# Performance work log

Hardware: AMD Instinct MI355X
Metric: run time of the kernel (lower is better)

Reference implementation:

```python
import jax, jax.numpy as jnp
import numpy as np

B, N, W, R = 32, 1024, 128, 4
EPS = 1e-8  # torch CosineSimilarity eps


def _cosine(key, mem):
    # key: (B,K,W), mem: (B,N,W) -> (B,K,N); torch-style eps clamp on norm product
    dot = jnp.einsum('bkw,bnw->bkn', key, mem)
    kn = jnp.linalg.norm(key, axis=-1)[..., None]          # (B,K,1)
    mn = jnp.linalg.norm(mem, axis=-1)[:, None, :]          # (B,1,N)
    return dot / jnp.maximum(kn * mn, EPS)


def setup_inputs() -> dict:
    key = jax.random.key(0)
    ks = jax.random.split(key, 16)
    inp = {
        'memory': jax.random.normal(ks[0], (B, N, W), jnp.float32) * 0.1,
        'temporal_link': jax.random.uniform(ks[1], (B, N, N), jnp.float32) / N,
        'usage': jax.random.uniform(ks[2], (B, 1, N), jnp.float32),
        'precedence': jax.random.uniform(ks[3], (B, 1, N), jnp.float32) / N,
        'read_weights': jax.nn.softmax(jax.random.normal(ks[4], (B, R, N), jnp.float32), axis=-1),
        'read_keys': jax.random.normal(ks[5], (B, R, W), jnp.float32),
        'read_strength': 1.0 + jax.random.uniform(ks[6], (B, R, 1), jnp.float32),
        'read_modes': jax.nn.softmax(jax.random.normal(ks[7], (B, R, 3), jnp.float32), axis=-1),
        'write_key': jax.random.normal(ks[8], (B, W), jnp.float32),
        'write_strength': 1.0 + jax.random.uniform(ks[9], (B, 1), jnp.float32),
        'allocation_gate': jax.random.uniform(ks[10], (B, 1, 1), jnp.float32),
        'write_gate': jax.random.uniform(ks[11], (B, 1, 1), jnp.float32),
        'write_vector': jax.random.normal(ks[12], (B, 1, W), jnp.float32),
        'erase_vector': jax.random.uniform(ks[13], (B, 1, W), jnp.float32),
        'free_gates': jax.random.uniform(ks[14], (B, R, 1), jnp.float32),
    }
    return inp


def reference(memory, temporal_link, usage, precedence, read_weights,
              read_keys, read_strength, read_modes, write_key, write_strength,
              allocation_gate, write_gate, write_vector, erase_vector, free_gates):
    # --- read weights: temporal (fwd/bwd) + content modes ---
    # NOTE: source softmaxes the raw cosine, THEN multiplies by strength
    content_r = jax.nn.softmax(_cosine(read_keys, memory), axis=-1) * read_strength  # (B,R,N)
    fw = jnp.einsum('brn,bmn->brm', read_weights, temporal_link)   # rw @ L^T
    bw = jnp.einsum('brn,bnm->brm', read_weights, temporal_link)   # rw @ L
    new_rw = (fw * read_modes[:, :, 0:1] + bw * read_modes[:, :, 1:2]
              + content_r * read_modes[:, :, 2:3])                 # (B,R,N)
    read_result = jnp.einsum('brn,bnw->brw', new_rw, memory)       # (B,R,W)

    # --- allocation: exclusive cumprod of (unsorted) usage, as in source ---
    cp = jnp.cumprod(usage, axis=-1)
    excl = jnp.concatenate([jnp.ones_like(cp[..., :1]), cp[..., :-1]], axis=-1)
    allocation = (1.0 - usage) * excl                              # (B,1,N)

    # --- write weights (source multiplies strength BEFORE softmax here) ---
    wc = jax.nn.softmax(_cosine(write_key[:, None, :], memory)
                        * write_strength[:, :, None], axis=-1)     # (B,1,N)
    ww = (allocation_gate * (allocation - wc) + wc) * write_gate   # (B,1,N)
    wwT = jnp.swapaxes(ww, 1, 2)                                   # (B,N,1)

    # --- memory erase/write (outer products via broadcasting) ---
    memory_new = memory * (1.0 - wwT * erase_vector) + wwT * write_vector

    # --- temporal link update ---
    grid = wwT + ww                                                # (B,N,N)
    link_new = (1.0 - grid) * temporal_link + wwT * precedence     # (B,N,N)

    # NOTE: source uses a GLOBAL scalar sum of write weights here
    precedence_new = (1.0 - jnp.sum(ww)) * precedence + ww

    # --- usage update (source uses the freshly updated read weights) ---
    retention = jnp.prod(1.0 - free_gates * new_rw, axis=1, keepdims=True)  # (B,1,N)
    usage_new = (usage + ww - usage * ww) * retention

    return (read_result, memory_new, link_new, usage_new, precedence_new, new_rw)
```

## Files before the change

### kernel.cpp

```cpp
#include <hip/hip_runtime.h>
#include <math.h>

#define B 32
#define N 1024
#define W 128
#define R 4
#define EPSC 1e-8f

typedef float f32x4 __attribute__((ext_vector_type(4)));

#define WS_SUM   0
#define WS_BW    64
#define WS_FW    (WS_BW + B*16*R*N)
#define WS_CONT  (WS_FW + B*R*N)
#define WS_COSR  (WS_CONT + B*R*N)
#define WS_COSW  (WS_COSR + B*R*N)
#define WS_WW    (WS_COSW + B*N)

#define O_RR    0
#define O_MEM   (O_RR + B*R*W)
#define O_LINK  (O_MEM + B*N*W)
#define O_USAGE (O_LINK + B*N*N)
#define O_PREC  (O_USAGE + B*N)
#define O_NRW   (O_PREC + B*N)

__global__ void k1_scores(const float* __restrict__ mem,
                          const float* __restrict__ rkeys,
                          const float* __restrict__ wkey,
                          float* __restrict__ ws) {
    int bx = blockIdx.x;
    int b = bx >> 6;
    int n0 = (bx & 63) << 4;
    int t = threadIdx.x;
    __shared__ float keys[5][W];
    __shared__ float knorm[5];
    for (int idx = t; idx < 5 * W; idx += 256) {
        int r = idx >> 7, w = idx & 127;
        keys[r][w] = (r < 4) ? rkeys[(b * R + r) * W + w] : wkey[b * W + w];
    }
    __syncthreads();
    if (t < 160) {
        int kidx = t >> 5, l = t & 31;
        float s = 0.f;
        #pragma unroll
        for (int c = 0; c < 4; ++c) { float v = keys[kidx][l * 4 + c]; s += v * v; }
        #pragma unroll
        for (int st = 1; st <= 16; st <<= 1) s += __shfl_xor(s, st);
        if (l == 0) knorm[kidx] = sqrtf(s);
    }
    __syncthreads();
    int l16 = t & 15;
    int rloc = t >> 4;
    int n = n0 + rloc;
    const float* mrow = mem + ((size_t)(b * N + n)) * W + l16 * 8;
    float4 a  = *reinterpret_cast<const float4*>(mrow);
    float4 a2 = *reinterpret_cast<const float4*>(mrow + 4);
    float mm = a.x*a.x + a.y*a.y + a.z*a.z + a.w*a.w
             + a2.x*a2.x + a2.y*a2.y + a2.z*a2.z + a2.w*a2.w;
    float d[5];
    #pragma unroll
    for (int r = 0; r < 5; ++r) {
        float4 k1v = *reinterpret_cast<const float4*>(&keys[r][l16 * 8]);
        float4 k2v = *reinterpret_cast<const float4*>(&keys[r][l16 * 8 + 4]);
        d[r] = a.x*k1v.x + a.y*k1v.y + a.z*k1v.z + a.w*k1v.w
             + a2.x*k2v.x + a2.y*k2v.y + a2.z*k2v.z + a2.w*k2v.w;
    }
    #pragma unroll
    for (int st = 1; st <= 8; st <<= 1) {
        mm += __shfl_xor(mm, st);
        #pragma unroll
        for (int r = 0; r < 5; ++r) d[r] += __shfl_xor(d[r], st);
    }
    if (l16 == 0) {
        float mn = sqrtf(mm);
        #pragma unroll
        for (int r = 0; r < 4; ++r)
            ws[WS_COSR + (b * R + r) * N + n] = d[r] / fmaxf(knorm[r] * mn, EPSC);
        ws[WS_COSW + b * N + n] = d[4] / fmaxf(knorm[4] * mn, EPSC);
    }
}

__global__ void k2_soft(const float* __restrict__ usage,
                        const float* __restrict__ rstr,
                        const float* __restrict__ wstr,
                        const float* __restrict__ agate,
                        const float* __restrict__ wgate,
                        float* __restrict__ ws) {
    int b = blockIdx.x, t = threadIdx.x;
    int lane = t & 63, wv = t >> 6;
    __shared__ float red[16][8];
    __shared__ float fin[8];
    __shared__ float wsc[16];

    float x[5], m[5];
    #pragma unroll
    for (int r = 0; r < R; ++r) x[r] = ws[WS_COSR + (b * R + r) * N + t];
    x[4] = ws[WS_COSW + b * N + t] * wstr[b];
    #pragma unroll
    for (int q = 0; q < 5; ++q) m[q] = x[q];
    #pragma unroll
    for (int s = 1; s <= 32; s <<= 1) {
        #pragma unroll
        for (int q = 0; q < 5; ++q) m[q] = fmaxf(m[q], __shfl_xor(m[q], s));
    }
    if (lane == 0) { for (int q = 0; q < 5; ++q) red[wv][q] = m[q]; }
    __syncthreads();
    if (t < 80) {
        int q = t >> 4, w16 = t & 15;
        float v = red[w16][q];
        #pragma unroll
        for (int s = 1; s <= 8; s <<= 1) v = fmaxf(v, __shfl_xor(v, s));
        if (w16 == 0) fin[q] = v;
    }
    __syncthreads();
    float e[5], sm[5];
    #pragma unroll
    for (int q = 0; q < 5; ++q) { e[q] = expf(x[q] - fin[q]); sm[q] = e[q]; }
    #pragma unroll
    for (int s = 1; s <= 32; s <<= 1) {
        #pragma unroll
        for (int q = 0; q < 5; ++q) sm[q] += __shfl_xor(sm[q], s);
    }
    __syncthreads();
    if (lane == 0) { for (int q = 0; q < 5; ++q) red[wv][q] = sm[q]; }
    __syncthreads();
    if (t < 80) {
        int q = t >> 4, w16 = t & 15;
        float v = red[w16][q];
        #pragma unroll
        for (int s = 1; s <= 8; s <<= 1) v += __shfl_xor(v, s);
        if (w16 == 0) fin[q] = v;
    }
    __syncthreads();
    #pragma unroll
    for (int r = 0; r < R; ++r)
        ws[WS_CONT + (b * R + r) * N + t] = e[r] / fin[r] * rstr[b * R + r];
    float wcv = e[4] / fin[4];

    float u = usage[b * N + t];
    float incl = u;
    #pragma unroll
    for (int s = 1; s <= 32; s <<= 1) {
        float up = __shfl_up(incl, s);
        if (lane >= s) incl *= up;
    }
    if (lane == 63) wsc[wv] = incl;
    __syncthreads();
    if (t < 16) {
        float v = wsc[t];
        #pragma unroll
        for (int s = 1; s <= 8; s <<= 1) {
            float up = __shfl_up(v, s);
            if (lane >= s) v *= up;
        }
        wsc[t] = v;
    }
    __syncthreads();
    float woff = (wv == 0) ? 1.f : wsc[wv - 1];
    float eu = __shfl_up(incl, 1);
    float excl = (lane == 0 ? 1.f : eu) * woff;
    float alloc = (1.f - u) * excl;

    float wwv = (agate[b] * (alloc - wcv) + wcv) * wgate[b];
    ws[WS_WW + b * N + t] = wwv;

    float s6 = wwv;
    #pragma unroll
    for (int s = 1; s <= 32; s <<= 1) s6 += __shfl_xor(s6, s);
    __syncthreads();
    if (lane == 0) red[wv][0] = s6;
    __syncthreads();
    if (t == 0) {
        float acc = 0.f;
        for (int w2 = 0; w2 < 16; ++w2) acc += red[w2][0];
        atomicAdd(&ws[WS_SUM], acc);
    }
}

__global__ void k3_link(const float* __restrict__ L,
                        const float* __restrict__ rw,
                        const float* __restrict__ prec,
                        float* __restrict__ ws,
                        float* __restrict__ out) {
    int bx = blockIdx.x;
    int b = bx >> 4;
    int strip = bx & 15;
    int i0 = strip << 6;
    int t = threadIdx.x;
    __shared__ float scratch[256][36];
    __shared__ float ww_row[64];
    __shared__ float rw_row[R][64];

    if (t < 64) ww_row[t] = ws[WS_WW + b * N + i0 + t];
    for (int idx = t; idx < R * 64; idx += 256) {
        int r = idx >> 6, i = idx & 63;
        rw_row[r][i] = rw[(b * R + r) * N + i0 + i];
    }
    __syncthreads();

    int j0 = 4 * t;
    float4 wwj = *reinterpret_cast<const float4*>(ws + WS_WW + b * N + j0);
    float4 pj  = *reinterpret_cast<const float4*>(prec + b * N + j0);
    float4 rwj[R];
    #pragma unroll
    for (int r = 0; r < R; ++r)
        rwj[r] = *reinterpret_cast<const float4*>(rw + (b * R + r) * N + j0);
    float4 bwa[R];
    #pragma unroll
    for (int r = 0; r < R; ++r) bwa[r] = make_float4(0.f, 0.f, 0.f, 0.f);

    const float* Lr = L + ((size_t)(b * N + i0)) * N + j0;
    float* Or = out + O_LINK + ((size_t)(b * N + i0)) * N + j0;

    int g = t >> 3, kk = t & 7;

    for (int batch = 0; batch < 8; ++batch) {
        float4 v[8];
        #pragma unroll
        for (int k = 0; k < 8; ++k)
            v[k] = *reinterpret_cast<const float4*>(Lr + (size_t)(batch * 8 + k) * N);

        float4 fwp[8];
        #pragma unroll
        for (int k = 0; k < 8; ++k) {
            int row = batch * 8 + k;
            float wi = ww_row[row];
            float c = 1.f - wi;
            f32x4 o;
            o.x = (c - wwj.x) * v[k].x + wi * pj.x;
            o.y = (c - wwj.y) * v[k].y + wi * pj.y;
            o.z = (c - wwj.z) * v[k].z + wi * pj.z;
            o.w = (c - wwj.w) * v[k].w + wi * pj.w;
            __builtin_nontemporal_store(o,
                reinterpret_cast<f32x4*>(Or + (size_t)row * N));
            float4 f;
            f.x = v[k].x*rwj[0].x + v[k].y*rwj[0].y + v[k].z*rwj[0].z + v[k].w*rwj[0].w;
            f.y = v[k].x*rwj[1].x + v[k].y*rwj[1].y + v[k].z*rwj[1].z + v[k].w*rwj[1].w;
            f.z = v[k].x*rwj[2].x + v[k].y*rwj[2].y + v[k].z*rwj[2].z + v[k].w*rwj[2].w;
            f.w = v[k].x*rwj[3].x + v[k].y*rwj[3].y + v[k].z*rwj[3].z + v[k].w*rwj[3].w;
            fwp[k] = f;
            #pragma unroll
            for (int r = 0; r < R; ++r) {
                float q = rw_row[r][row];
                bwa[r].x += q * v[k].x; bwa[r].y += q * v[k].y;
                bwa[r].z += q * v[k].z; bwa[r].w += q * v[k].w;
            }
        }

        #pragma unroll
        for (int k = 0; k < 8; ++k)
            *reinterpret_cast<float4*>(&scratch[t][k * 4]) = fwp[k];
        __syncthreads();
        float s = 0.f;
        #pragma unroll
        for (int m = 0; m < 32; ++m) s += scratch[kk + 8 * m][g];
        s += __shfl_xor(s, 1);
        s += __shfl_xor(s, 2);
        s += __shfl_xor(s, 4);
        if (kk == 0) {
            int rowk = g >> 2, r = g & 3;
            ws[WS_FW + (b * R + r) * N + i0 + batch * 8 + rowk] = s;
        }
        __syncthreads();
    }

    float* bwout = ws + WS_BW + (size_t)(b * 16 + strip) * R * N;
    #pragma unroll
    for (int r = 0; r < R; ++r)
        *reinterpret_cast<float4*>(bwout + r * N + j0) = bwa[r];
}

__global__ void k4_final(const float* __restrict__ mem,
                         const float* __restrict__ usage,
                         const float* __restrict__ prec,
                         const float* __restrict__ rmodes,
                         const float* __restrict__ fgates,
                         const float* __restrict__ ev,
                         const float* __restrict__ wvec,
                         float* __restrict__ ws,
                         float* __restrict__ out) {
    int bx = blockIdx.x;
    int b = bx >> 4;
    int n0 = (bx & 15) << 6;
    int t = threadIdx.x;
    __shared__ float nrw[R][64];
    __shared__ float wwl[64];
    __shared__ float rrl[2][R][W];

    {
        int r = t >> 6, nl = t & 63, n = n0 + nl;
        float bs = 0.f;
        #pragma unroll
        for (int tile = 0; tile < 16; ++tile)
            bs += ws[WS_BW + ((size_t)(b * 16 + tile) * R + r) * N + n];
        float fwv = ws[WS_FW + (b * R + r) * N + n];
        float cv  = ws[WS_CONT + (b * R + r) * N + n];
        float m0 = rmodes[(b * R + r) * 3 + 0];
        float m1 = rmodes[(b * R + r) * 3 + 1];
        float m2 = rmodes[(b * R + r) * 3 + 2];
        float v = fwv * m0 + bs * m1 + cv * m2;
        out[O_NRW + (b * R + r) * N + n] = v;
        nrw[r][nl] = v;
    }
    __syncthreads();

    if (t < 64) {
        int n = n0 + t;
        float ret = 1.f;
        #pragma unroll
        for (int r = 0; r < R; ++r) ret *= (1.f - fgates[b * R + r] * nrw[r][t]);
        float u = usage[b * N + n];
        float w = ws[WS_WW + b * N + n];
        out[O_USAGE + b * N + n] = (u + w - u * w) * ret;
        float S = ws[WS_SUM];
        out[O_PREC + b * N + n] = (1.f - S) * prec[b * N + n] + w;
        wwl[t] = w;
    }
    __syncthreads();

    int wi = t & 127, half = t >> 7;
    float er = ev[b * W + wi], wvv = wvec[b * W + wi];
    float acc[R] = {0.f, 0.f, 0.f, 0.f};
    for (int k = 0; k < 32; ++k) {
        int nl = half * 32 + k;
        int n = n0 + nl;
        size_t off = ((size_t)(b * N + n)) * W + wi;
        float m = mem[off];
        float wn = wwl[nl];
        out[O_MEM + off] = m * (1.f - wn * er) + wn * wvv;
        #pragma unroll
        for (int r = 0; r < R; ++r) acc[r] += nrw[r][nl] * m;
    }
    #pragma unroll
    for (int r = 0; r < R; ++r) rrl[half][r][wi] = acc[r];
    __syncthreads();
    for (int idx = t; idx < R * W; idx += 256) {
        int r = idx >> 7, w2 = idx & 127;
        atomicAdd(&out[O_RR + (b * R + r) * W + w2], rrl[0][r][w2] + rrl[1][r][w2]);
    }
}

extern "C" void kernel_launch(void* const* d_in, const int* in_sizes, int n_in,
                              void* d_out, int out_size, void* d_ws, size_t ws_size,
                              hipStream_t stream) {
    const float* mem    = (const float*)d_in[0];
    const float* L      = (const float*)d_in[1];
    const float* usage  = (const float*)d_in[2];
    const float* prec   = (const float*)d_in[3];
    const float* rw     = (const float*)d_in[4];
    const float* rkeys  = (const float*)d_in[5];
    const float* rstr   = (const float*)d_in[6];
    const float* rmodes = (const float*)d_in[7];
    const float* wkey   = (const float*)d_in[8];
    const float* wstr   = (const float*)d_in[9];
    const float* ag     = (const float*)d_in[10];
    const float* wg     = (const float*)d_in[11];
    const float* wv     = (const float*)d_in[12];
    const float* ev     = (const float*)d_in[13];
    const float* fg     = (const float*)d_in[14];
    float* out = (float*)d_out;
    float* ws  = (float*)d_ws;

    (void)hipMemsetAsync(ws, 0, 256, stream);
    (void)hipMemsetAsync(out, 0, (size_t)B * R * W * sizeof(float), stream);

    k1_scores<<<B * 64, 256, 0, stream>>>(mem, rkeys, wkey, ws);
    k2_soft<<<B, 1024, 0, stream>>>(usage, rstr, wstr, ag, wg, ws);
    k3_link<<<B * 16, 256, 0, stream>>>(L, rw, prec, ws, out);
    k4_final<<<B * 16, 256, 0, stream>>>(mem, usage, prec, rmodes, fg, ev, wv, ws, out);
}
```

Before: 78.34 us.

## Fold softmax exp and sums into score kernel; halve link strip height

The score kernel now exponentiates cosine scores directly and atomically accumulates per-batch softmax denominators. This removes the max/sum reductions from the single-block-per-batch softmax kernel, and the content-weight normalization moves into the final kernel. Separately, the link kernel uses 32-row strips, doubling its grid to improve occupancy at the cost of more partial backward sums to reduce. Dropping max subtraction relies on cosine values being bounded, so exp cannot overflow, and the float atomics make the summation order nondeterministic.

Result: slower. 89.13 us (+13.8%).

```diff
diff --git a/kernel.cpp b/kernel.cpp
--- a/kernel.cpp
+++ b/kernel.cpp
@@ -10,12 +10,12 @@
 typedef float f32x4 __attribute__((ext_vector_type(4)));
 
 #define WS_SUM   0
-#define WS_BW    64
-#define WS_FW    (WS_BW + B*16*R*N)
-#define WS_CONT  (WS_FW + B*R*N)
-#define WS_COSR  (WS_CONT + B*R*N)
-#define WS_COSW  (WS_COSR + B*R*N)
-#define WS_WW    (WS_COSW + B*N)
+#define WS_KSUM  64
+#define WS_BW    256
+#define WS_FW    (WS_BW + B*32*R*N)
+#define WS_ER    (WS_FW + B*R*N)
+#define WS_EW    (WS_ER + B*R*N)
+#define WS_WW    (WS_EW + B*N)
 
 #define O_RR    0
 #define O_MEM   (O_RR + B*R*W)
@@ -27,6 +27,7 @@
 __global__ void k1_scores(const float* __restrict__ mem,
                           const float* __restrict__ rkeys,
                           const float* __restrict__ wkey,
+                          const float* __restrict__ wstr,
                           float* __restrict__ ws) {
     int bx = blockIdx.x;
     int b = bx >> 6;
@@ -34,6 +35,7 @@
     int t = threadIdx.x;
     __shared__ float keys[5][W];
     __shared__ float knorm[5];
+    __shared__ float epart[5][16];
     for (int idx = t; idx < 5 * W; idx += 256) {
         int r = idx >> 7, w = idx & 127;
         keys[r][w] = (r < 4) ? rkeys[(b * R + r) * W + w] : wkey[b * W + w];
@@ -73,69 +75,40 @@
     }
     if (l16 == 0) {
         float mn = sqrtf(mm);
-        #pragma unroll
-        for (int r = 0; r < 4; ++r)
-            ws[WS_COSR + (b * R + r) * N + n] = d[r] / fmaxf(knorm[r] * mn, EPSC);
-        ws[WS_COSW + b * N + n] = d[4] / fmaxf(knorm[4] * mn, EPSC);
+        float e[5];
+        #pragma unroll
+        for (int r = 0; r < 4; ++r) {
+            float c = d[r] / fmaxf(knorm[r] * mn, EPSC);
+            e[r] = expf(c);
+            ws[WS_ER + (b * R + r) * N + n] = e[r];
+        }
+        float cw = d[4] / fmaxf(knorm[4] * mn, EPSC);
+        e[4] = expf(cw * wstr[b]);
+        ws[WS_EW + b * N + n] = e[4];
+        #pragma unroll
+        for (int q = 0; q < 5; ++q) epart[q][rloc] = e[q];
+    }
+    __syncthreads();
+    if (t < 80) {
+        int q = t >> 4, i = t & 15;
+        float v = epart[q][i];
+        #pragma unroll
+        for (int st = 1; st <= 8; st <<= 1) v += __shfl_xor(v, st);
+        if (i == 0) atomicAdd(&ws[WS_KSUM + b * 5 + q], v);
     }
 }
 
 __global__ void k2_soft(const float* __restrict__ usage,
-                        const float* __restrict__ rstr,
-                        const float* __restrict__ wstr,
                         const float* __restrict__ agate,
                         const float* __restrict__ wgate,
                         float* __restrict__ ws) {
     int b = blockIdx.x, t = threadIdx.x;
     int lane = t & 63, wv = t >> 6;
-    __shared__ float red[16][8];
-    __shared__ float fin[8];
     __shared__ float wsc[16];
-
-    float x[5], m[5];
-    #pragma unroll
-    for (int r = 0; r < R; ++r) x[r] = ws[WS_COSR + (b * R + r) * N + t];
-    x[4] = ws[WS_COSW + b * N + t] * wstr[b];
-    #pragma unroll
-    for (int q = 0; q < 5; ++q) m[q] = x[q];
-    #pragma unroll
-    for (int s = 1; s <= 32; s <<= 1) {
-        #pragma unroll
-        for (int q = 0; q < 5; ++q) m[q] = fmaxf(m[q], __shfl_xor(m[q], s));
-    }
-    if (lane == 0) { for (int q = 0; q < 5; ++q) red[wv][q] = m[q]; }
-    __syncthreads();
-    if (t < 80) {
-        int q = t >> 4, w16 = t & 15;
-        float v = red[w16][q];
-        #pragma unroll
-        for (int s = 1; s <= 8; s <<= 1) v = fmaxf(v, __shfl_xor(v, s));
-        if (w16 == 0) fin[q] = v;
-    }
-    __syncthreads();
-    float e[5], sm[5];
-    #pragma unroll
-    for (int q = 0; q < 5; ++q) { e[q] = expf(x[q] - fin[q]); sm[q] = e[q]; }
-    #pragma unroll
-    for (int s = 1; s <= 32; s <<= 1) {
-        #pragma unroll
-        for (int q = 0; q < 5; ++q) sm[q] += __shfl_xor(sm[q], s);
-    }
-    __syncthreads();
-    if (lane == 0) { for (int q = 0; q < 5; ++q) red[wv][q] = sm[q]; }
-    __syncthreads();
-    if (t < 80) {
-        int q = t >> 4, w16 = t & 15;
-        float v = red[w16][q];
-        #pragma unroll
-        for (int s = 1; s <= 8; s <<= 1) v += __shfl_xor(v, s);
-        if (w16 == 0) fin[q] = v;
-    }
-    __syncthreads();
-    #pragma unroll
-    for (int r = 0; r < R; ++r)
-        ws[WS_CONT + (b * R + r) * N + t] = e[r] / fin[r] * rstr[b * R + r];
-    float wcv = e[4] / fin[4];
+    __shared__ float red[16];
+
+    float sw = ws[WS_KSUM + b * 5 + 4];
+    float wcv = ws[WS_EW + b * N + t] / sw;
 
     float u = usage[b * N + t];
     float incl = u;
@@ -168,11 +141,11 @@
     #pragma unroll
     for (int s = 1; s <= 32; s <<= 1) s6 += __shfl_xor(s6, s);
     __syncthreads();
-    if (lane == 0) red[wv][0] = s6;
+    if (lane == 0) red[wv] = s6;
     __syncthreads();
     if (t == 0) {
         float acc = 0.f;
-        for (int w2 = 0; w2 < 16; ++w2) acc += red[w2][0];
+        for (int w2 = 0; w2 < 16; ++w2) acc += red[w2];
         atomicAdd(&ws[WS_SUM], acc);
     }
 }
@@ -183,17 +156,18 @@
                         float* __restrict__ ws,
                         float* __restrict__ out) {
     int bx = blockIdx.x;
-    int b = bx >> 4;
-    int strip = bx & 15;
-    int i0 = strip << 6;
+    int b = bx >> 5;
+    int strip = bx & 31;
+    int i0 = strip << 5;
     int t = threadIdx.x;
     __shared__ float scratch[256][36];
-    __shared__ float ww_row[64];
-    __shared__ float rw_row[R][64];
-
-    if (t < 64) ww_row[t] = ws[WS_WW + b * N + i0 + t];
-    for (int idx = t; idx < R * 64; idx += 256) {
-        int r = idx >> 6, i = idx & 63;
+    __shared__ float ww_row[32];
+    __shared__ float rw_row[R][32];
+
+    if (t < 32) ww_row[t] = ws[WS_WW + b * N + i0 + t];
+    if (t >= 64 && t < 192) {
+        int idx = t - 64;
+        int r = idx >> 5, i = idx & 31;
         rw_row[r][i] = rw[(b * R + r) * N + i0 + i];
     }
     __syncthreads();
@@ -214,7 +188,7 @@
 
     int g = t >> 3, kk = t & 7;
 
-    for (int batch = 0; batch < 8; ++batch) {
+    for (int batch = 0; batch < 4; ++batch) {
         float4 v[8];
         #pragma unroll
         for (int k = 0; k < 8; ++k)
@@ -264,7 +238,7 @@
         __syncthreads();
     }
 
-    float* bwout = ws + WS_BW + (size_t)(b * 16 + strip) * R * N;
+    float* bwout = ws + WS_BW + (size_t)(b * 32 + strip) * R * N;
     #pragma unroll
     for (int r = 0; r < R; ++r)
         *reinterpret_cast<float4*>(bwout + r * N + j0) = bwa[r];
@@ -274,6 +248,7 @@
                          const float* __restrict__ usage,
                          const float* __restrict__ prec,
                          const float* __restrict__ rmodes,
+                         const float* __restrict__ rstr,
                          const float* __restrict__ fgates,
                          const float* __restrict__ ev,
                          const float* __restrict__ wvec,
@@ -291,10 +266,11 @@
         int r = t >> 6, nl = t & 63, n = n0 + nl;
         float bs = 0.f;
         #pragma unroll
-        for (int tile = 0; tile < 16; ++tile)
-            bs += ws[WS_BW + ((size_t)(b * 16 + tile) * R + r) * N + n];
+        for (int tile = 0; tile < 32; ++tile)
+            bs += ws[WS_BW + ((size_t)(b * 32 + tile) * R + r) * N + n];
         float fwv = ws[WS_FW + (b * R + r) * N + n];
-        float cv  = ws[WS_CONT + (b * R + r) * N + n];
+        float cv  = ws[WS_ER + (b * R + r) * N + n] / ws[WS_KSUM + b * 5 + r]
+                    * rstr[b * R + r];
         float m0 = rmodes[(b * R + r) * 3 + 0];
         float m1 = rmodes[(b * R + r) * 3 + 1];
         float m2 = rmodes[(b * R + r) * 3 + 2];
@@ -361,11 +337,11 @@
     float* out = (float*)d_out;
     float* ws  = (float*)d_ws;
 
-    (void)hipMemsetAsync(ws, 0, 256, stream);
+    (void)hipMemsetAsync(ws, 0, 1024, stream);
     (void)hipMemsetAsync(out, 0, (size_t)B * R * W * sizeof(float), stream);
 
-    k1_scores<<<B * 64, 256, 0, stream>>>(mem, rkeys, wkey, ws);
-    k2_soft<<<B, 1024, 0, stream>>>(usage, rstr, wstr, ag, wg, ws);
-    k3_link<<<B * 16, 256, 0, stream>>>(L, rw, prec, ws, out);
-    k4_final<<<B * 16, 256, 0, stream>>>(mem, usage, prec, rmodes, fg, ev, wv, ws, out);
-}
+    k1_scores<<<B * 64, 256, 0, stream>>>(mem, rkeys, wkey, wstr, ws);
+    k2_soft<<<B, 1024, 0, stream>>>(usage, ag, wg, ws);
+    k3_link<<<B * 32, 256, 0, stream>>>(L, rw, prec, ws, out);
+    k4_final<<<B * 16, 256, 0, stream>>>(mem, usage, prec, rmodes, rstr, fg, ev, wv, ws, out);
+}
```
